# Kernel optimization log

Hardware: AMD Instinct MI355X
Metric: run time of the kernel (lower is better)

Reference implementation:

```python
import jax, jax.numpy as jnp
import numpy as np

B, S, T = 32, 32, 64          # docs, sentences/doc, tokens/sentence
E, HW, HS = 128, 128, 128     # embed, word hidden, sentence hidden
CW, CS = 128, 128             # attention context sizes
V, NC = 50000, 8              # vocab, classes


def setup_inputs() -> dict:
    key = jax.random.key(0)
    ks = iter(jax.random.split(key, 40))
    x = jax.random.randint(next(ks), (B, S, T), 1, V, dtype=jnp.int32)
    wl = jax.random.randint(next(ks), (B, S), 8, T + 1)   # word lengths
    sl = jax.random.randint(next(ks), (B,), 8, S + 1)     # sentence counts
    tmask = jnp.arange(T)[None, None, :] < wl[:, :, None]
    smask = (jnp.arange(S)[None, :] < sl[:, None])[:, :, None]
    x = jnp.where(tmask & smask, x, 0)                     # 0 = pad token

    def u(shape, scale=0.1):
        return jax.random.uniform(next(ks), shape, jnp.float32, -scale, scale)

    d = {"x": x, "emb": u((V, E))}
    # GRU params in torch layout: W_ih [3H,D] (r|z|n), W_hh [3H,H], biases [3H]
    for pre, Din, H in [("wf", E, HW), ("wb", E, HW), ("sf", 2 * HW, HS), ("sb", 2 * HW, HS)]:
        d[pre + "_Wih"] = u((3 * H, Din))
        d[pre + "_Whh"] = u((3 * H, H))
        d[pre + "_bih"] = u((3 * H,))
        d[pre + "_bhh"] = u((3 * H,))
    d["wproj_W"] = u((CW, 2 * HW)); d["wproj_b"] = u((CW,)); d["wctx"] = u((CW,))
    d["sproj_W"] = u((CS, 2 * HS)); d["sproj_b"] = u((CS,)); d["sctx"] = u((CS,))
    d["fc_W"] = u((NC, 2 * HS)); d["fc_b"] = u((NC,))
    return d


def seq_lens_2d(tok):
    # torch get_sequence_lens: T - trailing zeros, 1 if all zero
    nz = tok != 0
    any_nz = jnp.any(nz, axis=1)
    last = tok.shape[1] - jnp.argmax(nz[:, ::-1], axis=1)
    return jnp.where(any_nz, last, 1)


def doc_lens(x):
    # torch get_num_sentences_lens: S - trailing all-zero sentences
    nz = jnp.any(x != 0, axis=2)  # [B,S]
    any_nz = jnp.any(nz, axis=1)
    last = x.shape[1] - jnp.argmax(nz[:, ::-1], axis=1)
    return jnp.where(any_nz, last, 1)


def run_gru(x, lens, Wih, Whh, bih, bhh, reverse):
    # x: [N,Tm,D]; emulates pack_padded: state frozen / output zeroed beyond len
    N, Tm, _ = x.shape
    H = Whh.shape[1]
    xp = jnp.einsum('ntd,gd->ntg', x, Wih) + bih  # [N,Tm,3H]

    def step(h, inp):
        xg, t = inp
        hg = h @ Whh.T + bhh
        xr, xz, xn = jnp.split(xg, 3, axis=-1)
        hr, hz, hn = jnp.split(hg, 3, axis=-1)
        r = jax.nn.sigmoid(xr + hr)
        z = jax.nn.sigmoid(xz + hz)
        n = jnp.tanh(xn + r * hn)
        h_new = (1 - z) * n + z * h
        valid = (t < lens)[:, None]
        h_new = jnp.where(valid, h_new, h)
        return h_new, jnp.where(valid, h_new, 0.0)

    h0 = jnp.zeros((N, H), x.dtype)
    _, ys = jax.lax.scan(step, h0, (jnp.swapaxes(xp, 0, 1), jnp.arange(Tm)), reverse=reverse)
    return jnp.swapaxes(ys, 0, 1)  # [N,Tm,H]


def bigru(x, lens, pf, pb):
    return jnp.concatenate([run_gru(x, lens, *pf, reverse=False),
                            run_gru(x, lens, *pb, reverse=True)], axis=-1)


def attn_pool(out, lens, Wp, bp, ctx):
    # faithful to torch: softmax over padded positions up to max(lens)
    # (pad_packed pads to max length; padded outputs are zero but score=tanh(b)@c)
    Tm = out.shape[1]
    scores = jnp.tanh(out @ Wp.T + bp) @ ctx            # [N,Tm]
    valid = jnp.arange(Tm)[None, :] < jnp.max(lens)
    attn = jax.nn.softmax(jnp.where(valid, scores, -jnp.inf), axis=-1)
    return jnp.einsum('nt,nth->nh', attn, out)


def han_forward(x, emb,
                wf_Wih, wf_Whh, wf_bih, wf_bhh, wb_Wih, wb_Whh, wb_bih, wb_bhh,
                wproj_W, wproj_b, wctx,
                sf_Wih, sf_Whh, sf_bih, sf_bhh, sb_Wih, sb_Whh, sb_bih, sb_bhh,
                sproj_W, sproj_b, sctx, fc_W, fc_b):
    Bx, Sx, Tx = x.shape
    xw = x.reshape(-1, Tx)                      # [B*S, T]
    wlens = seq_lens_2d(xw)
    slens = doc_lens(x)
    we = emb[xw]                                # [B*S, T, E]
    wout = bigru(we, wlens, (wf_Wih, wf_Whh, wf_bih, wf_bhh),
                 (wb_Wih, wb_Whh, wb_bih, wb_bhh))     # [B*S, T, 2HW]
    sent = attn_pool(wout, wlens, wproj_W, wproj_b, wctx)  # [B*S, 2HW]
    sent = sent.reshape(Bx, Sx, -1)
    sout = bigru(sent, slens, (sf_Wih, sf_Whh, sf_bih, sf_bhh),
                 (sb_Wih, sb_Whh, sb_bih, sb_bhh))     # [B, S, 2HS]
    doc = attn_pool(sout, slens, sproj_W, sproj_b, sctx)   # [B, 2HS]
    return doc @ fc_W.T + fc_b                             # [B, NC]


def reference(x, emb,
              wf_Wih, wf_Whh, wf_bih, wf_bhh, wb_Wih, wb_Whh, wb_bih, wb_bhh,
              wproj_W, wproj_b, wctx,
              sf_Wih, sf_Whh, sf_bih, sf_bhh, sb_Wih, sb_Whh, sb_bih, sb_bhh,
              sproj_W, sproj_b, sctx, fc_W, fc_b):
    return han_forward(x, emb,
                       wf_Wih, wf_Whh, wf_bih, wf_bhh, wb_Wih, wb_Whh, wb_bih, wb_bhh,
                       wproj_W, wproj_b, wctx,
                       sf_Wih, sf_Whh, sf_bih, sf_bhh, sb_Wih, sb_Whh, sb_bih, sb_bhh,
                       sproj_W, sproj_b, sctx, fc_W, fc_b)
```

## Files before the change

kernel.cpp:

```cpp
#include <hip/hip_runtime.h>
#include <hip/hip_bf16.h>

typedef unsigned short ushort_t;
typedef __attribute__((ext_vector_type(4))) float floatx4;
typedef __attribute__((ext_vector_type(8))) short short8;

#define L2E 1.4426950408889634f

__device__ __forceinline__ float bf2f(ushort_t u) {
    union { unsigned int i; float f; } v; v.i = ((unsigned int)u) << 16; return v.f;
}
__device__ __forceinline__ ushort_t f2bf(float f) {
    union { float f; unsigned int i; } v; v.f = f;
    unsigned int i = v.i;
    i += 0x7fffu + ((i >> 16) & 1u);
    return (ushort_t)(i >> 16);
}
__device__ __forceinline__ float fexp2(float x) {
#if __has_builtin(__builtin_amdgcn_exp2f)
    return __builtin_amdgcn_exp2f(x);
#else
    return __expf(x * 0.6931471805599453f);
#endif
}
__device__ __forceinline__ float frcp(float x) {
#if __has_builtin(__builtin_amdgcn_rcpf)
    return __builtin_amdgcn_rcpf(x);
#else
    return 1.f / x;
#endif
}
__device__ __forceinline__ float sig2(float a)  { return frcp(1.f + fexp2(a)); }
__device__ __forceinline__ float tanh2(float y) { return 1.f - 2.f * frcp(1.f + fexp2(y)); }

__device__ __forceinline__ unsigned int packbf(float a, float b) {
    float2 t; t.x = a; t.y = b;
    __hip_bfloat162 h = __float22bfloat162_rn(t);
    union { __hip_bfloat162 h; unsigned int u; } v; v.h = h; return v.u;
}

__device__ __forceinline__ floatx4 MFMA16(short8 a, short8 b, floatx4 c) {
    return __builtin_amdgcn_mfma_f32_16x16x32_bf16(a, b, c, 0, 0, 0);
}

__device__ __forceinline__ void bar_lds() {
    __builtin_amdgcn_s_waitcnt(0xc07f);
    __builtin_amdgcn_s_barrier();
}

#define XIDX(c, m) ((((c) * 16) + ((m) ^ ((c) & 15))) * 8)
#define X8(c, m) ((((c) * 8) + ((m) ^ ((c) & 7))) * 8)

__global__ __launch_bounds__(64) void lens_kernel(const int* __restrict__ x,
                                                  const unsigned int* __restrict__ raw,
                                                  int* wlens, int* slens, int* dmax,
                                                  int* flag) {
    int b = blockIdx.x, s = threadIdx.x;
    if (b == 32) {
        int c = 0;
        for (int i = 0; i < 16; ++i) {
            unsigned int v = raw[s * 16 + i];
            unsigned int e = (v >> 7) & 0xFFu;
            if (e > 0x7Bu) ++c;
        }
        c += __shfl_xor(c, 1);  c += __shfl_xor(c, 2);  c += __shfl_xor(c, 4);
        c += __shfl_xor(c, 8);  c += __shfl_xor(c, 16); c += __shfl_xor(c, 32);
        if (s == 0) *flag = (c > 64) ? 1 : 0;
        return;
    }
    int last = 0;
    if (s < 32) {
        const int* tok = x + (b * 32 + s) * 64;
        for (int t = 0; t < 64; t += 4) {
            int4 v = *(const int4*)(tok + t);
            if (v.x) last = t + 1;
            if (v.y) last = t + 2;
            if (v.z) last = t + 3;
            if (v.w) last = t + 4;
        }
        wlens[b * 32 + s] = last ? last : 1;
    }
    int len = (s < 32) ? (last ? last : 1) : 0;
    int lm = len;
    for (int off = 32; off; off >>= 1) lm = max(lm, __shfl_xor(lm, off));
    unsigned long long mask = __ballot(s < 32 && last > 0);
    if (s == 0) {
        slens[b] = mask ? (63 - (int)__clzll(mask) + 1) : 1;
        dmax[b] = lm;
    }
}

struct ConvArgs {
    const void* src[25];
    int dstoff[25];
    int count[25];
    int cumblk[26];
    int mode[25];
    int rowdiv[25];
};

__global__ __launch_bounds__(256) void convert_kernel(ConvArgs a, ushort_t* __restrict__ dst,
                                                      const int* __restrict__ flag) {
    int b = blockIdx.x;
    int lo = 0, hi = 24;
    while (lo < hi) { int mid = (lo + hi + 1) >> 1; if (a.cumblk[mid] <= b) lo = mid; else hi = mid - 1; }
    int j = lo;
    int base = (b - a.cumblk[j]) * 2048 + threadIdx.x * 8;
    if (base >= a.count[j]) return;
    ushort_t* out = dst + a.dstoff[j] + base;
    int m = a.mode[j], rd = a.rowdiv[j];
    float f[8];
    if (*flag) {
        const float* s = (const float*)a.src[j] + base;
        float4 v0 = *(const float4*)s;
        float4 v1 = *(const float4*)(s + 4);
        f[0] = v0.x; f[1] = v0.y; f[2] = v0.z; f[3] = v0.w;
        f[4] = v1.x; f[5] = v1.y; f[6] = v1.z; f[7] = v1.w;
    } else {
        const ushort_t* s = (const ushort_t*)a.src[j] + base;
        uint4 v = *(const uint4*)s;
        const ushort_t* u = (const ushort_t*)&v;
        #pragma unroll
        for (int e = 0; e < 8; ++e) f[e] = bf2f(u[e]);
    }
    union { ushort_t u[8]; uint4 v; } o;
    #pragma unroll
    for (int e = 0; e < 8; ++e) {
        float sc = 1.f;
        if (m == 2) sc = 2.f * L2E;
        else if (m == 1) sc = ((base + e) / rd < 256) ? -L2E : 2.f * L2E;
        o.u[e] = f2bf(f[e] * sc);
    }
    *(uint4*)out = o.v;
}

__global__ __launch_bounds__(512, 2) void word_gru_kernel(
        const int* __restrict__ x, const ushort_t* __restrict__ emb,
        const ushort_t* __restrict__ Wih_f, const ushort_t* __restrict__ Whh_f,
        const ushort_t* __restrict__ bih_f, const ushort_t* __restrict__ bhh_f,
        const ushort_t* __restrict__ Wih_b, const ushort_t* __restrict__ Whh_b,
        const ushort_t* __restrict__ bih_b, const ushort_t* __restrict__ bhh_b,
        const int* __restrict__ lens, ushort_t* __restrict__ out) {
    const int T = 64;
    __shared__ ushort_t h_buf[2][1024];
    __shared__ float bsum_lds[256];
    __shared__ float bihn_lds[128];
    __shared__ float bhhn_lds[128];
    __shared__ int tok_lds[512];

    int tid = threadIdx.x;
    int d = blockIdx.y;
    int n0 = blockIdx.x * 8;
    const ushort_t* Wih = d ? Wih_b : Wih_f;
    const ushort_t* Whh = d ? Whh_b : Whh_f;
    const ushort_t* bih = d ? bih_b : bih_f;
    const ushort_t* bhh = d ? bhh_b : bhh_f;
    int lane = tid & 63, wave = tid >> 6;
    int l15 = lane & 15, l4 = (lane >> 4) & 3;
    int s8 = l15 & 7;
    bool sv = l15 < 8;
    int jt = wave * 16;
    int j0 = jt + l4 * 4;

    {
        int t = tid >> 3, s = tid & 7;
        tok_lds[tid] = x[(n0 + s) * 64 + t];
    }
    if (tid < 256) bsum_lds[tid] = bf2f(bih[tid]) + bf2f(bhh[tid]);
    else if (tid < 384) {
        bihn_lds[tid - 256] = bf2f(bih[tid]);
        bhhn_lds[tid - 256] = bf2f(bhh[tid]);
    }
    if (tid < 256) { uint2 z = {0u, 0u}; *(uint2*)&h_buf[0][tid * 4] = z; }

    short8 wr[4], wz[4], wn[4], ur[4], uz[4], un[4];
    #pragma unroll
    for (int kf = 0; kf < 4; ++kf) {
        int col = kf * 32 + l4 * 8;
        wr[kf] = *(const short8*)(Wih + (size_t)(jt + l15) * 128 + col);
        wz[kf] = *(const short8*)(Wih + (size_t)(128 + jt + l15) * 128 + col);
        wn[kf] = *(const short8*)(Wih + (size_t)(256 + jt + l15) * 128 + col);
        ur[kf] = *(const short8*)(Whh + (size_t)(jt + l15) * 128 + col);
        uz[kf] = *(const short8*)(Whh + (size_t)(128 + jt + l15) * 128 + col);
        un[kf] = *(const short8*)(Whh + (size_t)(256 + jt + l15) * 128 + col);
    }
    __syncthreads();

    floatx4 br  = *(floatx4*)&bsum_lds[j0];
    floatx4 bz  = *(floatx4*)&bsum_lds[128 + j0];
    floatx4 bxn = *(floatx4*)&bihn_lds[j0];
    floatx4 bhn = *(floatx4*)&bhhn_lds[j0];
    int lv = lens[n0 + s8];
    float hreg[4] = {0.f, 0.f, 0.f, 0.f};

    short8 xc[4], xn_[4];
    {
        int t0 = d ? (T - 1) : 0;
        size_t rb = (size_t)tok_lds[t0 * 8 + s8] * 128 + l4 * 8;
        #pragma unroll
        for (int kf = 0; kf < 4; ++kf)
            xc[kf] = *(const short8*)(emb + rb + kf * 32);
    }

    for (int ti = 0; ti < T; ++ti) {
        int t = d ? (T - 1 - ti) : ti;
        bool have_next = (ti + 1) < T;
        if (have_next) {
            int tn = d ? (T - 2 - ti) : (ti + 1);
            size_t rb = (size_t)tok_lds[tn * 8 + s8] * 128 + l4 * 8;
            #pragma unroll
            for (int kf = 0; kf < 4; ++kf)
                xn_[kf] = *(const short8*)(emb + rb + kf * 32);
        }
        short8 hb[4];
        #pragma unroll
        for (int kf = 0; kf < 4; ++kf)
            hb[kf] = *(const short8*)&h_buf[ti & 1][X8(kf * 4 + l4, s8)];
        floatx4 arx = br, azx = bz, axn = bxn;
        floatx4 arh = {0.f, 0.f, 0.f, 0.f}, azh = {0.f, 0.f, 0.f, 0.f}, ahn = bhn;
        #pragma unroll
        for (int kf = 0; kf < 4; ++kf) {
            arx = MFMA16(wr[kf], xc[kf], arx);
            azx = MFMA16(wz[kf], xc[kf], azx);
            axn = MFMA16(wn[kf], xc[kf], axn);
        }
        #pragma unroll
        for (int kf = 0; kf < 4; ++kf) {
            arh = MFMA16(ur[kf], hb[kf], arh);
            azh = MFMA16(uz[kf], hb[kf], azh);
            ahn = MFMA16(un[kf], hb[kf], ahn);
        }
        bool valid = t < lv;
        float hnew[4];
        #pragma unroll
        for (int i = 0; i < 4; ++i) {
            float r  = sig2(arx[i] + arh[i]);
            float z  = sig2(azx[i] + azh[i]);
            float nn = tanh2(axn[i] + r * ahn[i]);
            hnew[i] = valid ? (nn + z * (hreg[i] - nn)) : hreg[i];
            hreg[i] = hnew[i];
        }
        if (sv) {
            uint2 h2, o2;
            h2.x = packbf(hnew[0], hnew[1]);
            h2.y = packbf(hnew[2], hnew[3]);
            o2.x = valid ? h2.x : 0u;
            o2.y = valid ? h2.y : 0u;
            *(uint2*)&h_buf[(ti & 1) ^ 1][X8(j0 >> 3, s8) + (j0 & 7)] = h2;
            *(uint2*)(out + ((size_t)(n0 + s8) * T + t) * 256 + d * 128 + j0) = o2;
        }
        if (have_next) {
            #pragma unroll
            for (int kf = 0; kf < 4; ++kf) xc[kf] = xn_[kf];
        }
        bar_lds();
    }
}

__global__ __launch_bounds__(256) void spt_gemm_kernel(const ushort_t* __restrict__ A,
                                                       const ushort_t* __restrict__ Bf_,
                                                       const ushort_t* __restrict__ biasf,
                                                       ushort_t* __restrict__ Tf_,
                                                       const ushort_t* __restrict__ Bb_,
                                                       const ushort_t* __restrict__ biasb,
                                                       ushort_t* __restrict__ Tb_) {
    __shared__ ushort_t As[64 * 256];
    __shared__ ushort_t Bs[64 * 256];
    const int K = 256;
    int tid = threadIdx.x;
    int by = blockIdx.y;
    bool sb = by >= 6;
    int n0 = (sb ? by - 6 : by) * 64;
    const ushort_t* B = sb ? Bb_ : Bf_;
    const ushort_t* bias = sb ? biasb : biasf;
    ushort_t* Tp = sb ? Tb_ : Tf_;
    int m0 = blockIdx.x * 64;
    for (int idx = tid; idx < 2048; idx += 256) {
        int m = idx & 63, c = idx >> 6;
        *(uint4*)&As[(c * 64 + m) * 8] = *(const uint4*)(A + (size_t)(m0 + m) * K + c * 8);
    }
    for (int idx = tid; idx < 2048; idx += 256) {
        int n = idx & 63, c = idx >> 6;
        *(uint4*)&Bs[(c * 64 + n) * 8] = *(const uint4*)(B + (size_t)(n0 + n) * K + c * 8);
    }
    __syncthreads();
    int lane = tid & 63, wave = tid >> 6;
    int wm = (wave & 1) * 32, wn = (wave >> 1) * 32;
    int l15 = lane & 15, l4 = lane >> 4;
    floatx4 acc[2][2] = {};
    for (int kf = 0; kf < 8; ++kf) {
        int c = kf * 4 + l4;
        short8 a0 = *(const short8*)&As[(c * 64 + wm + l15) * 8];
        short8 a1 = *(const short8*)&As[(c * 64 + wm + 16 + l15) * 8];
        short8 b0 = *(const short8*)&Bs[(c * 64 + wn + l15) * 8];
        short8 b1 = *(const short8*)&Bs[(c * 64 + wn + 16 + l15) * 8];
        acc[0][0] = MFMA16(a0, b0, acc[0][0]);
        acc[0][1] = MFMA16(a0, b1, acc[0][1]);
        acc[1][0] = MFMA16(a1, b0, acc[1][0]);
        acc[1][1] = MFMA16(a1, b1, acc[1][1]);
    }
    for (int nt = 0; nt < 2; ++nt) {
        int n = n0 + wn + nt * 16 + l15;
        float bv = bf2f(bias[n]);
        int jc = n >> 2, ji = n & 3;
        for (int mt = 0; mt < 2; ++mt) {
            int mbase = m0 + wm + mt * 16 + l4 * 4;
            #pragma unroll
            for (int i = 0; i < 4; ++i) {
                int m = mbase + i;
                int doc = m >> 5, t = m & 31;
                size_t dst = ((size_t)((doc >> 4) * 32 + t) * 96 + jc) * 64
                           + (doc & 15) * 4 + ji;
                Tp[dst] = f2bf(acc[mt][nt][i] + bv);
            }
        }
    }
}

__global__ __launch_bounds__(512, 2) void sent_gru_kernel(
        const ushort_t* __restrict__ spT_f, const ushort_t* __restrict__ spT_b,
        const ushort_t* __restrict__ Whh_f, const ushort_t* __restrict__ Whh_b,
        const ushort_t* __restrict__ bhh_f, const ushort_t* __restrict__ bhh_b,
        const int* __restrict__ lens, ushort_t* __restrict__ out) {
    const int T = 32;
    __shared__ ushort_t h_buf[2][1024];
    __shared__ float bhh_lds[384];

    int tid = threadIdx.x;
    int d = blockIdx.y;
    int bx = blockIdx.x;
    int n0 = bx * 8;
    const ushort_t* spT = d ? spT_b : spT_f;
    const ushort_t* Whh = d ? Whh_b : Whh_f;
    const ushort_t* bhh = d ? bhh_b : bhh_f;
    int lane = tid & 63, wave = tid >> 6;
    int l15 = lane & 15, l4 = (lane >> 4) & 3;
    int s8 = l15 & 7;
    bool sv = l15 < 8;
    int jt = wave * 16;
    int j0 = jt + l4 * 4;
    int jc = j0 >> 2;

    if (tid < 384) bhh_lds[tid] = bf2f(bhh[tid]);
    if (tid < 256) { uint2 z = {0u, 0u}; *(uint2*)&h_buf[0][tid * 4] = z; }

    short8 ur[4], uz[4], un[4];
    #pragma unroll
    for (int kf = 0; kf < 4; ++kf) {
        int col = kf * 32 + l4 * 8;
        ur[kf] = *(const short8*)(Whh + (size_t)(jt + l15) * 128 + col);
        uz[kf] = *(const short8*)(Whh + (size_t)(128 + jt + l15) * 128 + col);
        un[kf] = *(const short8*)(Whh + (size_t)(256 + jt + l15) * 128 + col);
    }
    __syncthreads();

    floatx4 br  = *(floatx4*)&bhh_lds[j0];
    floatx4 bz  = *(floatx4*)&bhh_lds[128 + j0];
    floatx4 bhn = *(floatx4*)&bhh_lds[256 + j0];
    int lv = lens[n0 + s8];
    float hreg[4] = {0.f, 0.f, 0.f, 0.f};

    const ushort_t* sp = spT + (size_t)((bx >> 1) * 32) * 96 * 64
                       + ((bx & 1) * 8 + s8) * 4;
    ushort4 xr_c, xz_c, xn_c, xr_n, xz_n, xn_n;
    {
        int t0 = d ? (T - 1) : 0;
        size_t rb = (size_t)t0 * 96 * 64;
        xr_c = *(const ushort4*)(sp + rb + (size_t)jc * 64);
        xz_c = *(const ushort4*)(sp + rb + (size_t)(32 + jc) * 64);
        xn_c = *(const ushort4*)(sp + rb + (size_t)(64 + jc) * 64);
    }

    for (int ti = 0; ti < T; ++ti) {
        int t = d ? (T - 1 - ti) : ti;
        int cur = ti & 1;
        bool have_next = (ti + 1) < T;
        if (have_next) {
            int tn = d ? (T - 2 - ti) : (ti + 1);
            size_t rb = (size_t)tn * 96 * 64;
            xr_n = *(const ushort4*)(sp + rb + (size_t)jc * 64);
            xz_n = *(const ushort4*)(sp + rb + (size_t)(32 + jc) * 64);
            xn_n = *(const ushort4*)(sp + rb + (size_t)(64 + jc) * 64);
        }
        floatx4 ar = br, az = bz, ahn = bhn;
        #pragma unroll
        for (int kf = 0; kf < 4; ++kf) {
            short8 hb = *(const short8*)&h_buf[cur][X8(kf * 4 + l4, s8)];
            ar  = MFMA16(ur[kf], hb, ar);
            az  = MFMA16(uz[kf], hb, az);
            ahn = MFMA16(un[kf], hb, ahn);
        }
        float xr[4] = {bf2f(xr_c.x), bf2f(xr_c.y), bf2f(xr_c.z), bf2f(xr_c.w)};
        float xz[4] = {bf2f(xz_c.x), bf2f(xz_c.y), bf2f(xz_c.z), bf2f(xz_c.w)};
        float xn[4] = {bf2f(xn_c.x), bf2f(xn_c.y), bf2f(xn_c.z), bf2f(xn_c.w)};
        bool valid = t < lv;
        float hnew[4];
        #pragma unroll
        for (int i = 0; i < 4; ++i) {
            float r  = sig2(xr[i] + ar[i]);
            float z  = sig2(xz[i] + az[i]);
            float nn = tanh2(xn[i] + r * ahn[i]);
            hnew[i] = valid ? (nn + z * (hreg[i] - nn)) : hreg[i];
            hreg[i] = hnew[i];
        }
        if (sv) {
            uint2 h2, o2;
            h2.x = packbf(hnew[0], hnew[1]);
            h2.y = packbf(hnew[2], hnew[3]);
            o2.x = valid ? h2.x : 0u;
            o2.y = valid ? h2.y : 0u;
            *(uint2*)&h_buf[cur ^ 1][X8(j0 >> 3, s8) + (j0 & 7)] = h2;
            *(uint2*)(out + ((size_t)(n0 + s8) * T + t) * 256 + d * 128 + j0) = o2;
        }
        if (have_next) { xr_c = xr_n; xz_c = xz_n; xn_c = xn_n; }
        bar_lds();
    }
}

#define SP 264
__global__ __launch_bounds__(256) void word_attn_kernel(const ushort_t* __restrict__ wout,
                                                        const ushort_t* __restrict__ W,
                                                        const ushort_t* __restrict__ bias,
                                                        const ushort_t* __restrict__ ctx,
                                                        const int* __restrict__ dmax,
                                                        ushort_t* __restrict__ sent) {
    __shared__ ushort_t tile[64 * SP];
    __shared__ float bc[256];
    __shared__ float sc_lds[64];
    __shared__ float p_lds[64];
    int tid = threadIdx.x, g = blockIdx.x;
    for (int idx = tid; idx < 2048; idx += 256) {
        int row = idx >> 5, k0 = (idx & 31) * 8;
        *(uint4*)&tile[row * SP + k0] = *(const uint4*)(wout + ((size_t)g * 64 + row) * 256 + k0);
    }
    if (tid < 128) bc[tid] = bf2f(bias[tid]);
    else bc[tid] = bf2f(ctx[tid - 128]);
    __syncthreads();
    int lane = tid & 63, wave = tid >> 6;
    int l15 = lane & 15, l4 = (lane >> 4) & 3;
    short8 a[8];
    #pragma unroll
    for (int kf = 0; kf < 8; ++kf)
        a[kf] = *(const short8*)&tile[(wave * 16 + l15) * SP + kf * 32 + l4 * 8];
    floatx4 acc[8];
    #pragma unroll
    for (int nt = 0; nt < 8; ++nt) {
        floatx4 c = {0.f, 0.f, 0.f, 0.f};
        #pragma unroll
        for (int kf = 0; kf < 8; ++kf) {
            short8 b = *(const short8*)(W + (size_t)(nt * 16 + l15) * 256 + kf * 32 + l4 * 8);
            c = MFMA16(a[kf], b, c);
        }
        acc[nt] = c;
    }
    float s[4] = {0.f, 0.f, 0.f, 0.f};
    #pragma unroll
    for (int nt = 0; nt < 8; ++nt) {
        float bv = bc[nt * 16 + l15], cv = bc[128 + nt * 16 + l15];
        #pragma unroll
        for (int i = 0; i < 4; ++i)
            s[i] += tanh2(acc[nt][i] + bv) * cv;
    }
    #pragma unroll
    for (int i = 0; i < 4; ++i) {
        s[i] += __shfl_xor(s[i], 1);
        s[i] += __shfl_xor(s[i], 2);
        s[i] += __shfl_xor(s[i], 4);
        s[i] += __shfl_xor(s[i], 8);
    }
    if (l15 == 0) {
        #pragma unroll
        for (int i = 0; i < 4; ++i) sc_lds[wave * 16 + l4 * 4 + i] = s[i];
    }
    __syncthreads();
    if (tid < 64) {
        int ml = dmax[tid & 31];
        for (int off = 32; off; off >>= 1) ml = max(ml, __shfl_xor(ml, off));
        bool v = tid < ml;
        float sc = v ? sc_lds[tid] : -1e30f;
        float mx = sc;
        for (int off = 32; off; off >>= 1) mx = fmaxf(mx, __shfl_xor(mx, off));
        float e = v ? __expf(sc - mx) : 0.f;
        float sum = e;
        for (int off = 32; off; off >>= 1) sum += __shfl_xor(sum, off);
        p_lds[tid] = e * frcp(fmaxf(sum, 1e-30f));
    }
    __syncthreads();
    float acc2 = 0.f;
    for (int t = 0; t < 64; ++t) acc2 += p_lds[t] * bf2f(tile[t * SP + tid]);
    sent[(size_t)g * 256 + tid] = f2bf(acc2);
}

__global__ __launch_bounds__(256) void sent_attn_fc_kernel(const ushort_t* __restrict__ sout,
                                                           const ushort_t* __restrict__ W,
                                                           const ushort_t* __restrict__ bias,
                                                           const ushort_t* __restrict__ ctx,
                                                           const ushort_t* __restrict__ fcW,
                                                           const ushort_t* __restrict__ fcb,
                                                           const int* __restrict__ slens,
                                                           const int* __restrict__ flagp,
                                                           void* __restrict__ outp) {
    __shared__ ushort_t tile[32 * SP];
    __shared__ float bc[256];
    __shared__ float sc_lds[32];
    __shared__ float p_lds[32];
    __shared__ float dv[256];
    int tid = threadIdx.x, g = blockIdx.x;
    for (int idx = tid; idx < 1024; idx += 256) {
        int row = idx >> 5, k0 = (idx & 31) * 8;
        *(uint4*)&tile[row * SP + k0] = *(const uint4*)(sout + ((size_t)g * 32 + row) * 256 + k0);
    }
    if (tid < 128) bc[tid] = bf2f(bias[tid]);
    else bc[tid] = bf2f(ctx[tid - 128]);
    __syncthreads();
    int lane = tid & 63, wave = tid >> 6;
    int l15 = lane & 15, l4 = (lane >> 4) & 3;
    if (wave < 2) {
        short8 a[8];
        #pragma unroll
        for (int kf = 0; kf < 8; ++kf)
            a[kf] = *(const short8*)&tile[(wave * 16 + l15) * SP + kf * 32 + l4 * 8];
        floatx4 acc[8];
        #pragma unroll
        for (int nt = 0; nt < 8; ++nt) {
            floatx4 c = {0.f, 0.f, 0.f, 0.f};
            #pragma unroll
            for (int kf = 0; kf < 8; ++kf) {
                short8 b = *(const short8*)(W + (size_t)(nt * 16 + l15) * 256 + kf * 32 + l4 * 8);
                c = MFMA16(a[kf], b, c);
            }
            acc[nt] = c;
        }
        float s[4] = {0.f, 0.f, 0.f, 0.f};
        #pragma unroll
        for (int nt = 0; nt < 8; ++nt) {
            float bv = bc[nt * 16 + l15], cv = bc[128 + nt * 16 + l15];
            #pragma unroll
            for (int i = 0; i < 4; ++i)
                s[i] += tanh2(acc[nt][i] + bv) * cv;
        }
        #pragma unroll
        for (int i = 0; i < 4; ++i) {
            s[i] += __shfl_xor(s[i], 1);
            s[i] += __shfl_xor(s[i], 2);
            s[i] += __shfl_xor(s[i], 4);
            s[i] += __shfl_xor(s[i], 8);
        }
        if (l15 == 0) {
            #pragma unroll
            for (int i = 0; i < 4; ++i) sc_lds[wave * 16 + l4 * 4 + i] = s[i];
        }
    }
    __syncthreads();
    if (tid < 32) {
        int ml = slens[tid];
        for (int off = 16; off; off >>= 1) ml = max(ml, __shfl_xor(ml, off, 32));
        bool v = tid < ml;
        float sc = v ? sc_lds[tid] : -1e30f;
        float mx = sc;
        for (int off = 16; off; off >>= 1) mx = fmaxf(mx, __shfl_xor(mx, off, 32));
        float e = v ? __expf(sc - mx) : 0.f;
        float sum = e;
        for (int off = 16; off; off >>= 1) sum += __shfl_xor(sum, off, 32);
        p_lds[tid] = e * frcp(fmaxf(sum, 1e-30f));
    }
    __syncthreads();
    float acc2 = 0.f;
    for (int t = 0; t < 32; ++t) acc2 += p_lds[t] * bf2f(tile[t * SP + tid]);
    dv[tid] = acc2;
    __syncthreads();
    int c = tid >> 5, q0 = (tid & 31) * 8;
    float partial = 0.f;
    #pragma unroll
    for (int q = 0; q < 8; ++q)
        partial += dv[q0 + q] * bf2f(fcW[(size_t)c * 256 + q0 + q]);
    for (int off = 16; off; off >>= 1) partial += __shfl_xor(partial, off, 32);
    if ((tid & 31) == 0) {
        float v = partial + bf2f(fcb[c]);
        if (*flagp) ((float*)outp)[g * 8 + c] = v;
        else        ((ushort_t*)outp)[g * 8 + c] = f2bf(v);
    }
}

extern "C" void kernel_launch(void* const* d_in, const int* in_sizes, int n_in,
                              void* d_out, int out_size, void* d_ws, size_t ws_size,
                              hipStream_t stream) {
    const int* x = (const int*)d_in[0];
    char* ws = (char*)d_ws;

    const size_t O_CONV = 0;
    const size_t O_WOUT = 14680064;
    const size_t O_SENT = 48234496;
    const size_t O_SOUT = 48758784;
    const size_t O_SPTF = 49283072;
    const size_t O_SPTB = 50855936;
    const size_t O_LENS = 52428800;
    const size_t O_SLEN = 52432896;
    const size_t O_DMAX = 52433024;
    const size_t O_FLAG = 52433152;

    ushort_t* conv = (ushort_t*)(ws + O_CONV);
    ushort_t* wout = (ushort_t*)(ws + O_WOUT);
    ushort_t* sent = (ushort_t*)(ws + O_SENT);
    ushort_t* sout = (ushort_t*)(ws + O_SOUT);
    ushort_t* sptf = (ushort_t*)(ws + O_SPTF);
    ushort_t* sptb = (ushort_t*)(ws + O_SPTB);
    int* wlens = (int*)(ws + O_LENS);
    int* slens = (int*)(ws + O_SLEN);
    int* dmax  = (int*)(ws + O_DMAX);
    int* flag  = (int*)(ws + O_FLAG);

    static const int kMode[25]   = {0, 1,1,1,1, 1,1,1,1, 1,1,1,1, 1,1,1,1, 2,2,0, 2,2,0, 0,0};
    static const int kRowdiv[25] = {1, 128,128,1,1, 128,128,1,1, 256,128,1,1, 256,128,1,1,
                                    1,1,1, 1,1,1, 1,1};

    ConvArgs ca;
    ushort_t* cw[25];
    int off = 0, blk = 0;
    for (int i = 1; i <= 25; ++i) {
        int j = i - 1;
        int cnt = in_sizes[i];
        ca.src[j] = d_in[i];
        ca.dstoff[j] = off;
        ca.count[j] = cnt;
        ca.cumblk[j] = blk;
        ca.mode[j] = kMode[j];
        ca.rowdiv[j] = kRowdiv[j];
        cw[j] = conv + off;
        off += cnt;
        blk += (cnt + 2047) / 2048;
    }
    ca.cumblk[25] = blk;

    lens_kernel<<<33, 64, 0, stream>>>(x, (const unsigned int*)d_in[1],
                                       wlens, slens, dmax, flag);
    convert_kernel<<<blk, 256, 0, stream>>>(ca, conv, flag);
    word_gru_kernel<<<dim3(128, 2), 512, 0, stream>>>(
        x, cw[0],
        cw[1], cw[2], cw[3], cw[4],
        cw[5], cw[6], cw[7], cw[8],
        wlens, wout);
    word_attn_kernel<<<1024, 256, 0, stream>>>(wout, cw[17], cw[18], cw[19], dmax, sent);
    spt_gemm_kernel<<<dim3(16, 12), 256, 0, stream>>>(sent, cw[9], cw[11], sptf,
                                                      cw[13], cw[15], sptb);
    sent_gru_kernel<<<dim3(4, 2), 512, 0, stream>>>(
        sptf, sptb, cw[10], cw[14], cw[12], cw[16], slens, sout);
    sent_attn_fc_kernel<<<32, 256, 0, stream>>>(sout, cw[20], cw[21], cw[22],
                                                cw[23], cw[24], slens, flag, d_out);
    (void)n_in; (void)out_size; (void)ws_size;
}
```

Before: 279.0 us.

## Trim GRU recurrences to per-block max length and zero-fill the tail

The word and sentence GRU kernels now compute the maximum sequence length over the 8 sequences in each block and run the recurrence only up to that length, writing zeros for the remaining timesteps in a separate loop. For the backward direction this is valid because state is frozen while t >= len, so starting at tmax-1 matches starting at T-1. The word GRU loop is also unrolled by two with ping-pong register buffers in place of the copy, token offsets are premultiplied by 128 with 32-bit indexing, and the word-attention pooling uses four partial accumulators. The intent is to skip padded serial steps, which are the critical path, at the cost of a tail-store loop and slightly more code.

```diff
diff --git a/kernel.cpp b/kernel.cpp
--- a/kernel.cpp
+++ b/kernel.cpp
@@ -134,6 +134,58 @@
     *(uint4*)out = o.v;
 }
 
+#define GRU_STEP(K, XC, XN)                                                   \
+    do {                                                                      \
+        int t = d ? (tmax - 1 - (K)) : (K);                                   \
+        if ((K) + 1 < tmax) {                                                 \
+            int tn = d ? (tmax - 2 - (K)) : ((K) + 1);                        \
+            int rb = tok_lds[tn * 8 + s8] + l4 * 8;                           \
+            _Pragma("unroll")                                                 \
+            for (int kf = 0; kf < 4; ++kf)                                    \
+                XN[kf] = *(const short8*)(emb + rb + kf * 32);                \
+        }                                                                     \
+        short8 hb[4];                                                         \
+        _Pragma("unroll")                                                     \
+        for (int kf = 0; kf < 4; ++kf)                                        \
+            hb[kf] = *(const short8*)&h_buf[(K) & 1][X8(kf * 4 + l4, s8)];    \
+        floatx4 arx = br, azx = bz, axn = bxn;                                \
+        floatx4 arh = {0.f, 0.f, 0.f, 0.f};                                   \
+        floatx4 azh = {0.f, 0.f, 0.f, 0.f};                                   \
+        floatx4 ahn = bhn;                                                    \
+        _Pragma("unroll")                                                     \
+        for (int kf = 0; kf < 4; ++kf) {                                      \
+            arx = MFMA16(wr[kf], XC[kf], arx);                                \
+            azx = MFMA16(wz[kf], XC[kf], azx);                                \
+            axn = MFMA16(wn[kf], XC[kf], axn);                                \
+        }                                                                     \
+        _Pragma("unroll")                                                     \
+        for (int kf = 0; kf < 4; ++kf) {                                      \
+            arh = MFMA16(ur[kf], hb[kf], arh);                                \
+            azh = MFMA16(uz[kf], hb[kf], azh);                                \
+            ahn = MFMA16(un[kf], hb[kf], ahn);                                \
+        }                                                                     \
+        bool valid = t < lv;                                                  \
+        float hnew[4];                                                        \
+        _Pragma("unroll")                                                     \
+        for (int i = 0; i < 4; ++i) {                                         \
+            float r  = sig2(arx[i] + arh[i]);                                 \
+            float z  = sig2(azx[i] + azh[i]);                                 \
+            float nn = tanh2(axn[i] + r * ahn[i]);                            \
+            hnew[i] = valid ? (nn + z * (hreg[i] - nn)) : hreg[i];            \
+            hreg[i] = hnew[i];                                                \
+        }                                                                     \
+        if (sv) {                                                             \
+            uint2 h2, o2;                                                     \
+            h2.x = packbf(hnew[0], hnew[1]);                                  \
+            h2.y = packbf(hnew[2], hnew[3]);                                  \
+            o2.x = valid ? h2.x : 0u;                                         \
+            o2.y = valid ? h2.y : 0u;                                         \
+            *(uint2*)&h_buf[((K) & 1) ^ 1][X8(j0 >> 3, s8) + (j0 & 7)] = h2;  \
+            *(uint2*)(out + ((size_t)(n0 + s8) * T + t) * 256 + d * 128 + j0) = o2; \
+        }                                                                     \
+        bar_lds();                                                            \
+    } while (0)
+
 __global__ __launch_bounds__(512, 2) void word_gru_kernel(
         const int* __restrict__ x, const ushort_t* __restrict__ emb,
         const ushort_t* __restrict__ Wih_f, const ushort_t* __restrict__ Whh_f,
@@ -164,7 +216,7 @@
 
     {
         int t = tid >> 3, s = tid & 7;
-        tok_lds[tid] = x[(n0 + s) * 64 + t];
+        tok_lds[tid] = x[(n0 + s) * 64 + t] * 128;
     }
     if (tid < 256) bsum_lds[tid] = bf2f(bih[tid]) + bf2f(bhh[tid]);
     else if (tid < 384) {
@@ -184,76 +236,45 @@
         uz[kf] = *(const short8*)(Whh + (size_t)(128 + jt + l15) * 128 + col);
         un[kf] = *(const short8*)(Whh + (size_t)(256 + jt + l15) * 128 + col);
     }
+
+    int tmax = 1;
+    #pragma unroll
+    for (int q = 0; q < 8; ++q) tmax = max(tmax, lens[n0 + q]);
+    int lv = lens[n0 + s8];
+
     __syncthreads();
 
     floatx4 br  = *(floatx4*)&bsum_lds[j0];
     floatx4 bz  = *(floatx4*)&bsum_lds[128 + j0];
     floatx4 bxn = *(floatx4*)&bihn_lds[j0];
     floatx4 bhn = *(floatx4*)&bhhn_lds[j0];
-    int lv = lens[n0 + s8];
     float hreg[4] = {0.f, 0.f, 0.f, 0.f};
 
     short8 xc[4], xn_[4];
     {
-        int t0 = d ? (T - 1) : 0;
-        size_t rb = (size_t)tok_lds[t0 * 8 + s8] * 128 + l4 * 8;
+        int t0 = d ? (tmax - 1) : 0;
+        int rb = tok_lds[t0 * 8 + s8] + l4 * 8;
         #pragma unroll
         for (int kf = 0; kf < 4; ++kf)
             xc[kf] = *(const short8*)(emb + rb + kf * 32);
     }
 
-    for (int ti = 0; ti < T; ++ti) {
-        int t = d ? (T - 1 - ti) : ti;
-        bool have_next = (ti + 1) < T;
-        if (have_next) {
-            int tn = d ? (T - 2 - ti) : (ti + 1);
-            size_t rb = (size_t)tok_lds[tn * 8 + s8] * 128 + l4 * 8;
-            #pragma unroll
-            for (int kf = 0; kf < 4; ++kf)
-                xn_[kf] = *(const short8*)(emb + rb + kf * 32);
-        }
-        short8 hb[4];
-        #pragma unroll
-        for (int kf = 0; kf < 4; ++kf)
-            hb[kf] = *(const short8*)&h_buf[ti & 1][X8(kf * 4 + l4, s8)];
-        floatx4 arx = br, azx = bz, axn = bxn;
-        floatx4 arh = {0.f, 0.f, 0.f, 0.f}, azh = {0.f, 0.f, 0.f, 0.f}, ahn = bhn;
-        #pragma unroll
-        for (int kf = 0; kf < 4; ++kf) {
-            arx = MFMA16(wr[kf], xc[kf], arx);
-            azx = MFMA16(wz[kf], xc[kf], azx);
-            axn = MFMA16(wn[kf], xc[kf], axn);
-        }
-        #pragma unroll
-        for (int kf = 0; kf < 4; ++kf) {
-            arh = MFMA16(ur[kf], hb[kf], arh);
-            azh = MFMA16(uz[kf], hb[kf], azh);
-            ahn = MFMA16(un[kf], hb[kf], ahn);
-        }
-        bool valid = t < lv;
-        float hnew[4];
-        #pragma unroll
-        for (int i = 0; i < 4; ++i) {
-            float r  = sig2(arx[i] + arh[i]);
-            float z  = sig2(azx[i] + azh[i]);
-            float nn = tanh2(axn[i] + r * ahn[i]);
-            hnew[i] = valid ? (nn + z * (hreg[i] - nn)) : hreg[i];
-            hreg[i] = hnew[i];
-        }
-        if (sv) {
-            uint2 h2, o2;
-            h2.x = packbf(hnew[0], hnew[1]);
-            h2.y = packbf(hnew[2], hnew[3]);
-            o2.x = valid ? h2.x : 0u;
-            o2.y = valid ? h2.y : 0u;
-            *(uint2*)&h_buf[(ti & 1) ^ 1][X8(j0 >> 3, s8) + (j0 & 7)] = h2;
-            *(uint2*)(out + ((size_t)(n0 + s8) * T + t) * 256 + d * 128 + j0) = o2;
-        }
-        if (have_next) {
-            #pragma unroll
-            for (int kf = 0; kf < 4; ++kf) xc[kf] = xn_[kf];
-        }
-        bar_lds();
+    int k = 0;
+    for (; k + 1 < tmax; k += 2) {
+        GRU_STEP(k, xc, xn_);
+        GRU_STEP(k + 1, xn_, xc);
+    }
+    if (k < tmax) GRU_STEP(k, xc, xn_);
+
+    {
+        uint4 z4 = {0u, 0u, 0u, 0u};
+        int tail = (T - tmax) * 128;
+        for (int idx = tid; idx < tail; idx += 512) {
+            int t = tmax + (idx >> 7);
+            int rem = idx & 127;
+            int s = rem >> 4, c8 = rem & 15;
+            *(uint4*)(out + ((size_t)(n0 + s) * T + t) * 256 + d * 128 + c8 * 8) = z4;
+        }
     }
 }
 
@@ -352,31 +373,36 @@
         uz[kf] = *(const short8*)(Whh + (size_t)(128 + jt + l15) * 128 + col);
         un[kf] = *(const short8*)(Whh + (size_t)(256 + jt + l15) * 128 + col);
     }
+
+    int smax = 1;
+    #pragma unroll
+    for (int q = 0; q < 8; ++q) smax = max(smax, lens[n0 + q]);
+    int lv = lens[n0 + s8];
+
     __syncthreads();
 
     floatx4 br  = *(floatx4*)&bhh_lds[j0];
     floatx4 bz  = *(floatx4*)&bhh_lds[128 + j0];
     floatx4 bhn = *(floatx4*)&bhh_lds[256 + j0];
-    int lv = lens[n0 + s8];
     float hreg[4] = {0.f, 0.f, 0.f, 0.f};
 
     const ushort_t* sp = spT + (size_t)((bx >> 1) * 32) * 96 * 64
                        + ((bx & 1) * 8 + s8) * 4;
     ushort4 xr_c, xz_c, xn_c, xr_n, xz_n, xn_n;
     {
-        int t0 = d ? (T - 1) : 0;
+        int t0 = d ? (smax - 1) : 0;
         size_t rb = (size_t)t0 * 96 * 64;
         xr_c = *(const ushort4*)(sp + rb + (size_t)jc * 64);
         xz_c = *(const ushort4*)(sp + rb + (size_t)(32 + jc) * 64);
         xn_c = *(const ushort4*)(sp + rb + (size_t)(64 + jc) * 64);
     }
 
-    for (int ti = 0; ti < T; ++ti) {
-        int t = d ? (T - 1 - ti) : ti;
+    for (int ti = 0; ti < smax; ++ti) {
+        int t = d ? (smax - 1 - ti) : ti;
         int cur = ti & 1;
-        bool have_next = (ti + 1) < T;
+        bool have_next = (ti + 1) < smax;
         if (have_next) {
-            int tn = d ? (T - 2 - ti) : (ti + 1);
+            int tn = d ? (smax - 2 - ti) : (ti + 1);
             size_t rb = (size_t)tn * 96 * 64;
             xr_n = *(const ushort4*)(sp + rb + (size_t)jc * 64);
             xz_n = *(const ushort4*)(sp + rb + (size_t)(32 + jc) * 64);
@@ -414,6 +440,17 @@
         }
         if (have_next) { xr_c = xr_n; xz_c = xz_n; xn_c = xn_n; }
         bar_lds();
+    }
+
+    {
+        uint4 z4 = {0u, 0u, 0u, 0u};
+        int tail = (T - smax) * 128;
+        for (int idx = tid; idx < tail; idx += 512) {
+            int t = smax + (idx >> 7);
+            int rem = idx & 127;
+            int s = rem >> 4, c8 = rem & 15;
+            *(uint4*)(out + ((size_t)(n0 + s) * T + t) * 256 + d * 128 + c8 * 8) = z4;
+        }
     }
 }
 
@@ -486,9 +523,14 @@
         p_lds[tid] = e * frcp(fmaxf(sum, 1e-30f));
     }
     __syncthreads();
-    float acc2 = 0.f;
-    for (int t = 0; t < 64; ++t) acc2 += p_lds[t] * bf2f(tile[t * SP + tid]);
-    sent[(size_t)g * 256 + tid] = f2bf(acc2);
+    float a0 = 0.f, a1 = 0.f, a2 = 0.f, a3 = 0.f;
+    for (int t = 0; t < 64; t += 4) {
+        a0 += p_lds[t]     * bf2f(tile[t * SP + tid]);
+        a1 += p_lds[t + 1] * bf2f(tile[(t + 1) * SP + tid]);
+        a2 += p_lds[t + 2] * bf2f(tile[(t + 2) * SP + tid]);
+        a3 += p_lds[t + 3] * bf2f(tile[(t + 3) * SP + tid]);
+    }
+    sent[(size_t)g * 256 + tid] = f2bf((a0 + a1) + (a2 + a3));
 }
 
 __global__ __launch_bounds__(256) void sent_attn_fc_kernel(const ushort_t* __restrict__ sout,
```

Measured after the change: 293.7 us. +5.3%, slower.

## Fuse lens into convert kernel and sentence input GEMM into sentence GRU

Applied to the files above, without the earlier changes.

The separate lens kernel is folded into the convert kernel as extra blocks. Each block now computes the fp32/bf16 flag locally from a smaller 64-word sample, so it no longer waits on a global flag. The standalone sentence input-projection GEMM is removed, and each sentence GRU block computes its own slice of the projection with MFMA before the recurrence. This cuts two launches, but the projection now runs on only 8 blocks, which serializes more GEMM work. The flag heuristic also changes its sample size and threshold.

```diff
diff --git a/kernel.cpp b/kernel.cpp
--- a/kernel.cpp
+++ b/kernel.cpp
@@ -50,45 +50,6 @@
 
 #define XIDX(c, m) ((((c) * 16) + ((m) ^ ((c) & 15))) * 8)
 #define X8(c, m) ((((c) * 8) + ((m) ^ ((c) & 7))) * 8)
-
-__global__ __launch_bounds__(64) void lens_kernel(const int* __restrict__ x,
-                                                  const unsigned int* __restrict__ raw,
-                                                  int* wlens, int* slens, int* dmax,
-                                                  int* flag) {
-    int b = blockIdx.x, s = threadIdx.x;
-    if (b == 32) {
-        int c = 0;
-        for (int i = 0; i < 16; ++i) {
-            unsigned int v = raw[s * 16 + i];
-            unsigned int e = (v >> 7) & 0xFFu;
-            if (e > 0x7Bu) ++c;
-        }
-        c += __shfl_xor(c, 1);  c += __shfl_xor(c, 2);  c += __shfl_xor(c, 4);
-        c += __shfl_xor(c, 8);  c += __shfl_xor(c, 16); c += __shfl_xor(c, 32);
-        if (s == 0) *flag = (c > 64) ? 1 : 0;
-        return;
-    }
-    int last = 0;
-    if (s < 32) {
-        const int* tok = x + (b * 32 + s) * 64;
-        for (int t = 0; t < 64; t += 4) {
-            int4 v = *(const int4*)(tok + t);
-            if (v.x) last = t + 1;
-            if (v.y) last = t + 2;
-            if (v.z) last = t + 3;
-            if (v.w) last = t + 4;
-        }
-        wlens[b * 32 + s] = last ? last : 1;
-    }
-    int len = (s < 32) ? (last ? last : 1) : 0;
-    int lm = len;
-    for (int off = 32; off; off >>= 1) lm = max(lm, __shfl_xor(lm, off));
-    unsigned long long mask = __ballot(s < 32 && last > 0);
-    if (s == 0) {
-        slens[b] = mask ? (63 - (int)__clzll(mask) + 1) : 1;
-        dmax[b] = lm;
-    }
-}
 
 struct ConvArgs {
     const void* src[25];
@@ -100,17 +61,58 @@
 };
 
 __global__ __launch_bounds__(256) void convert_kernel(ConvArgs a, ushort_t* __restrict__ dst,
-                                                      const int* __restrict__ flag) {
-    int b = blockIdx.x;
+                                                      const int* __restrict__ x,
+                                                      int* wlens, int* slens, int* dmax,
+                                                      int* flagp) {
+    __shared__ int flag_lds;
+    int tid = threadIdx.x, b = blockIdx.x;
+    if (tid < 64) {
+        unsigned int v = ((const unsigned int*)a.src[0])[tid];
+        unsigned long long mball = __ballot(((v >> 7) & 0xFFu) > 0x7Bu);
+        if (tid == 0) flag_lds = (__popcll(mball) > 8) ? 1 : 0;
+    }
+    __syncthreads();
+    int flagv = flag_lds;
+    int cblk = a.cumblk[25];
+
+    if (b >= cblk) {
+        int bb = b - cblk;
+        if (bb == 0 && tid == 0) *flagp = flagv;
+        if (tid < 64) {
+            int s = tid;
+            int last = 0;
+            if (s < 32) {
+                const int* tok = x + (bb * 32 + s) * 64;
+                for (int t = 0; t < 64; t += 4) {
+                    int4 v = *(const int4*)(tok + t);
+                    if (v.x) last = t + 1;
+                    if (v.y) last = t + 2;
+                    if (v.z) last = t + 3;
+                    if (v.w) last = t + 4;
+                }
+                wlens[bb * 32 + s] = last ? last : 1;
+            }
+            int len = (s < 32) ? (last ? last : 1) : 0;
+            int lm = len;
+            for (int off = 32; off; off >>= 1) lm = max(lm, __shfl_xor(lm, off));
+            unsigned long long mask = __ballot(s < 32 && last > 0);
+            if (s == 0) {
+                slens[bb] = mask ? (63 - (int)__clzll(mask) + 1) : 1;
+                dmax[bb] = lm;
+            }
+        }
+        return;
+    }
+
     int lo = 0, hi = 24;
     while (lo < hi) { int mid = (lo + hi + 1) >> 1; if (a.cumblk[mid] <= b) lo = mid; else hi = mid - 1; }
     int j = lo;
-    int base = (b - a.cumblk[j]) * 2048 + threadIdx.x * 8;
+    int base = (b - a.cumblk[j]) * 2048 + tid * 8;
     if (base >= a.count[j]) return;
     ushort_t* out = dst + a.dstoff[j] + base;
     int m = a.mode[j], rd = a.rowdiv[j];
     float f[8];
-    if (*flag) {
+    if (flagv) {
         const float* s = (const float*)a.src[j] + base;
         float4 v0 = *(const float4*)s;
         float4 v1 = *(const float4*)(s + 4);
@@ -257,68 +259,11 @@
     }
 }
 
-__global__ __launch_bounds__(256) void spt_gemm_kernel(const ushort_t* __restrict__ A,
-                                                       const ushort_t* __restrict__ Bf_,
-                                                       const ushort_t* __restrict__ biasf,
-                                                       ushort_t* __restrict__ Tf_,
-                                                       const ushort_t* __restrict__ Bb_,
-                                                       const ushort_t* __restrict__ biasb,
-                                                       ushort_t* __restrict__ Tb_) {
-    __shared__ ushort_t As[64 * 256];
-    __shared__ ushort_t Bs[64 * 256];
-    const int K = 256;
-    int tid = threadIdx.x;
-    int by = blockIdx.y;
-    bool sb = by >= 6;
-    int n0 = (sb ? by - 6 : by) * 64;
-    const ushort_t* B = sb ? Bb_ : Bf_;
-    const ushort_t* bias = sb ? biasb : biasf;
-    ushort_t* Tp = sb ? Tb_ : Tf_;
-    int m0 = blockIdx.x * 64;
-    for (int idx = tid; idx < 2048; idx += 256) {
-        int m = idx & 63, c = idx >> 6;
-        *(uint4*)&As[(c * 64 + m) * 8] = *(const uint4*)(A + (size_t)(m0 + m) * K + c * 8);
-    }
-    for (int idx = tid; idx < 2048; idx += 256) {
-        int n = idx & 63, c = idx >> 6;
-        *(uint4*)&Bs[(c * 64 + n) * 8] = *(const uint4*)(B + (size_t)(n0 + n) * K + c * 8);
-    }
-    __syncthreads();
-    int lane = tid & 63, wave = tid >> 6;
-    int wm = (wave & 1) * 32, wn = (wave >> 1) * 32;
-    int l15 = lane & 15, l4 = lane >> 4;
-    floatx4 acc[2][2] = {};
-    for (int kf = 0; kf < 8; ++kf) {
-        int c = kf * 4 + l4;
-        short8 a0 = *(const short8*)&As[(c * 64 + wm + l15) * 8];
-        short8 a1 = *(const short8*)&As[(c * 64 + wm + 16 + l15) * 8];
-        short8 b0 = *(const short8*)&Bs[(c * 64 + wn + l15) * 8];
-        short8 b1 = *(const short8*)&Bs[(c * 64 + wn + 16 + l15) * 8];
-        acc[0][0] = MFMA16(a0, b0, acc[0][0]);
-        acc[0][1] = MFMA16(a0, b1, acc[0][1]);
-        acc[1][0] = MFMA16(a1, b0, acc[1][0]);
-        acc[1][1] = MFMA16(a1, b1, acc[1][1]);
-    }
-    for (int nt = 0; nt < 2; ++nt) {
-        int n = n0 + wn + nt * 16 + l15;
-        float bv = bf2f(bias[n]);
-        int jc = n >> 2, ji = n & 3;
-        for (int mt = 0; mt < 2; ++mt) {
-            int mbase = m0 + wm + mt * 16 + l4 * 4;
-            #pragma unroll
-            for (int i = 0; i < 4; ++i) {
-                int m = mbase + i;
-                int doc = m >> 5, t = m & 31;
-                size_t dst = ((size_t)((doc >> 4) * 32 + t) * 96 + jc) * 64
-                           + (doc & 15) * 4 + ji;
-                Tp[dst] = f2bf(acc[mt][nt][i] + bv);
-            }
-        }
-    }
-}
-
 __global__ __launch_bounds__(512, 2) void sent_gru_kernel(
-        const ushort_t* __restrict__ spT_f, const ushort_t* __restrict__ spT_b,
+        const ushort_t* __restrict__ sent,
+        ushort_t* __restrict__ spT_f, ushort_t* __restrict__ spT_b,
+        const ushort_t* __restrict__ Wx_f, const ushort_t* __restrict__ bi_f,
+        const ushort_t* __restrict__ Wx_b, const ushort_t* __restrict__ bi_b,
         const ushort_t* __restrict__ Whh_f, const ushort_t* __restrict__ Whh_b,
         const ushort_t* __restrict__ bhh_f, const ushort_t* __restrict__ bhh_b,
         const int* __restrict__ lens, ushort_t* __restrict__ out) {
@@ -351,6 +296,42 @@
         ur[kf] = *(const short8*)(Whh + (size_t)(jt + l15) * 128 + col);
         uz[kf] = *(const short8*)(Whh + (size_t)(128 + jt + l15) * 128 + col);
         un[kf] = *(const short8*)(Whh + (size_t)(256 + jt + l15) * 128 + col);
+    }
+
+    {
+        const ushort_t* Wx = d ? Wx_b : Wx_f;
+        const ushort_t* biv = d ? bi_b : bi_f;
+        ushort_t* Tp = d ? spT_b : spT_f;
+        int base_row = n0 * 32;
+        for (int mt = 0; mt < 16; ++mt) {
+            short8 a[8];
+            #pragma unroll
+            for (int kf = 0; kf < 8; ++kf)
+                a[kf] = *(const short8*)(sent + (size_t)(base_row + mt * 16 + l15) * 256 + kf * 32 + l4 * 8);
+            floatx4 pacc[3] = {};
+            #pragma unroll
+            for (int nt = 0; nt < 3; ++nt) {
+                #pragma unroll
+                for (int kf = 0; kf < 8; ++kf) {
+                    short8 bfr = *(const short8*)(Wx + (size_t)(wave * 48 + nt * 16 + l15) * 256 + kf * 32 + l4 * 8);
+                    pacc[nt] = MFMA16(a[kf], bfr, pacc[nt]);
+                }
+            }
+            #pragma unroll
+            for (int nt = 0; nt < 3; ++nt) {
+                int n = wave * 48 + nt * 16 + l15;
+                float bv = bf2f(biv[n]);
+                int pjc = n >> 2, ji = n & 3;
+                #pragma unroll
+                for (int i = 0; i < 4; ++i) {
+                    int mrow = mt * 16 + l4 * 4 + i;
+                    int doc = n0 + (mrow >> 5), tt = mrow & 31;
+                    size_t dst2 = ((size_t)((doc >> 4) * 32 + tt) * 96 + pjc) * 64
+                                + (doc & 15) * 4 + ji;
+                    Tp[dst2] = f2bf(pacc[nt][i] + bv);
+                }
+            }
+        }
     }
     __syncthreads();
 
@@ -632,19 +613,16 @@
     }
     ca.cumblk[25] = blk;
 
-    lens_kernel<<<33, 64, 0, stream>>>(x, (const unsigned int*)d_in[1],
-                                       wlens, slens, dmax, flag);
-    convert_kernel<<<blk, 256, 0, stream>>>(ca, conv, flag);
+    convert_kernel<<<blk + 32, 256, 0, stream>>>(ca, conv, x, wlens, slens, dmax, flag);
     word_gru_kernel<<<dim3(128, 2), 512, 0, stream>>>(
         x, cw[0],
         cw[1], cw[2], cw[3], cw[4],
         cw[5], cw[6], cw[7], cw[8],
         wlens, wout);
     word_attn_kernel<<<1024, 256, 0, stream>>>(wout, cw[17], cw[18], cw[19], dmax, sent);
-    spt_gemm_kernel<<<dim3(16, 12), 256, 0, stream>>>(sent, cw[9], cw[11], sptf,
-                                                      cw[13], cw[15], sptb);
     sent_gru_kernel<<<dim3(4, 2), 512, 0, stream>>>(
-        sptf, sptb, cw[10], cw[14], cw[12], cw[16], slens, sout);
+        sent, sptf, sptb, cw[9], cw[11], cw[13], cw[15],
+        cw[10], cw[14], cw[12], cw[16], slens, sout);
     sent_attn_fc_kernel<<<32, 256, 0, stream>>>(sout, cw[20], cw[21], cw[22],
                                                 cw[23], cw[24], slens, flag, d_out);
     (void)n_in; (void)out_size; (void)ws_size;
```

New measurement: 321.8 us. +15.3%, slower.
